# Kernel optimization log

Measured on AMD Instinct MI355X. Metric: run time of the kernel, lower is better.

The kernel has to match this reference:

```python
import jax, jax.numpy as jnp
import numpy as np

EPS = 1e-5

def _ln(x, g, b):
    mu = jnp.mean(x, -1, keepdims=True)
    var = jnp.mean(jnp.square(x - mu), -1, keepdims=True)
    return (x - mu) * jax.lax.rsqrt(var + EPS) * g + b

def _switch_moe(h, gw, gb, W1, b1, W2, b2):
    # h: [B,T,D]; top-1 switch routing over E experts
    probs = jax.nn.softmax(h @ gw + gb, axis=-1)        # [B,T,E]
    idx = jnp.argmax(probs, axis=-1)                    # [B,T]
    p = jnp.max(probs, axis=-1)[..., None]              # [B,T,1] top-1 gate prob
    out = jnp.zeros_like(h)
    E = W1.shape[0]
    for e in range(E):  # small fixed expert count
        y = jax.nn.gelu(h @ W1[e] + b1[e]) @ W2[e] + b2[e]
        out = out + jnp.where((idx == e)[..., None], p * y, 0.0)
    return out

def setup_inputs() -> dict:
    key = jax.random.key(0)
    B, T, D, F, E, TE, NB = 64, 196, 512, 2048, 8, 512, 2
    ks = jax.random.split(key, 16)
    s = 0.02
    return {
        "x": jax.random.normal(ks[0], (B, T, D), jnp.float32),
        "emb": jax.random.normal(ks[1], (B, TE), jnp.float32),
        "ln_g": jnp.ones((NB, D), jnp.float32),
        "ln_b": jnp.zeros((NB, D), jnp.float32),
        "gate_w": jax.random.normal(ks[2], (NB, D, E), jnp.float32) * s,
        "gate_b": jnp.zeros((NB, E), jnp.float32),
        "w1": jax.random.normal(ks[3], (NB, E, D, F), jnp.float32) * s,
        "b1": jnp.zeros((NB, E, F), jnp.float32),
        "w2": jax.random.normal(ks[4], (NB, E, F, D), jnp.float32) * s,
        "b2": jnp.zeros((NB, E, D), jnp.float32),
        "emb_w": jax.random.normal(ks[5], (TE, 2 * D), jnp.float32) * s,
        "emb_b": jnp.zeros((2 * D,), jnp.float32),
        "sn_g": jnp.ones((D,), jnp.float32),
        "sn_b": jnp.zeros((D,), jnp.float32),
        "out_w": jax.random.normal(ks[6], (D, D), jnp.float32) * s,
        "out_b": jnp.zeros((D,), jnp.float32),
    }

def reference(x, emb, ln_g, ln_b, gate_w, gate_b, w1, b1, w2, b2,
              emb_w, emb_b, sn_g, sn_b, out_w, out_b):
    NB = ln_g.shape[0]
    out = jnp.zeros_like(x)
    for br in range(NB):  # fixed small branch count; dropout = identity (eval)
        h = _ln(x, ln_g[br], ln_b[br])
        out = out + _switch_moe(h, gate_w[br], gate_b[br], w1[br], b1[br], w2[br], b2[br])
    out = out / NB
    # StylizationBlock (FiLM): norm, scale/shift from time emb, SiLU+Linear, residual
    eo = jax.nn.silu(emb) @ emb_w + emb_b            # [B,2D]
    scale, shift = jnp.split(eo[:, None, :], 2, axis=-1)  # [B,1,D] each
    h = _ln(out, sn_g, sn_b) * (1.0 + scale) + shift
    h = jax.nn.silu(h) @ out_w + out_b
    return x + h
```

## Files before the change

### kernel.cpp

```cpp
#include <hip/hip_runtime.h>
#include <hip/hip_bf16.h>

typedef unsigned short u16;
typedef unsigned int u32;

typedef short bf16v8 __attribute__((ext_vector_type(8)));
typedef float f32v4 __attribute__((ext_vector_type(4)));

constexpr int BB   = 64;
constexpr int TT   = 196;
constexpr int NTOK = BB * TT;
constexpr int DD   = 512;
constexpr int FF   = 2048;
constexpr int EE   = 8;
constexpr int NBR  = 2;
constexpr int GE   = NBR * EE;
constexpr int MT128 = 212;
constexpr int NB_FRONT = 8320 + NTOK / 4;

__device__ __forceinline__ u16 f2bf(float f) {
    union { float f; u32 u; } v; v.f = f;
    u32 r = v.u + 0x7fffu + ((v.u >> 16) & 1u);
    return (u16)(r >> 16);
}

__device__ __forceinline__ float bf2f(u32 u) {
    union { u32 u; float f; } v; v.u = u << 16; return v.f;
}

__device__ __forceinline__ float wave_sum(float v) {
    #pragma unroll
    for (int m = 32; m > 0; m >>= 1) v += __shfl_xor(v, m, 64);
    return v;
}

__device__ __forceinline__ float gelu_tanh(float v) {
    float y = 1.595769122f * v + 0.071354816f * (v * v * v);
    return v / (1.0f + __expf(-y));
}

__device__ __forceinline__ float silu(float v) {
    return v / (1.0f + __expf(-v));
}

__device__ __forceinline__ void gload16(const u16* g, u16* l) {
    typedef const __attribute__((address_space(1))) unsigned gv_t;
    typedef __attribute__((address_space(3))) unsigned lv_t;
    __builtin_amdgcn_global_load_lds((gv_t*)g, (lv_t*)l, 16, 0, 0);
}

__device__ __forceinline__ void bar() {
    asm volatile("" ::: "memory");
    __builtin_amdgcn_s_barrier();
    asm volatile("" ::: "memory");
}

#define ASM_VMCNT4 asm volatile("s_waitcnt vmcnt(4)" ::: "memory")
#define ASM_VMCNT0 asm volatile("s_waitcnt vmcnt(0)" ::: "memory")
#define ASM_LGKM0  asm volatile("s_waitcnt lgkmcnt(0)" ::: "memory")

__global__ __launch_bounds__(256) void front_kernel(
    const float* __restrict__ w1, u16* __restrict__ w1t,
    const float* __restrict__ w2, u16* __restrict__ w2t,
    const float* __restrict__ ow, u16* __restrict__ owt,
    const float* __restrict__ emb, const float* __restrict__ emb_w,
    const float* __restrict__ emb_b, float* __restrict__ eo,
    int* __restrict__ cnt,
    const float* __restrict__ x, const float* __restrict__ ln_g,
    const float* __restrict__ ln_b, const float* __restrict__ gate_w,
    const float* __restrict__ gate_b,
    u16* __restrict__ hA, u16* __restrict__ hB,
    int* __restrict__ idxb, float* __restrict__ pbuf)
{
    __shared__ float tile[64][69];
    __shared__ float se[4][DD];
    int id = blockIdx.x;
    int t = threadIdx.x;

    if (id >= 8320) {
        int wave = t >> 6, lane = t & 63;
        int tok = (id - 8320) * 4 + wave;
        const float* xr = x + (size_t)tok * DD + lane * 8;
        float4 v0 = *(const float4*)xr;
        float4 v1 = *(const float4*)(xr + 4);
        float xs[8] = {v0.x, v0.y, v0.z, v0.w, v1.x, v1.y, v1.z, v1.w};
        float s = 0.f, ss = 0.f;
        #pragma unroll
        for (int i = 0; i < 8; ++i) { s += xs[i]; ss += xs[i] * xs[i]; }
        s = wave_sum(s); ss = wave_sum(ss);
        float mu = s * (1.0f / DD);
        float var = ss * (1.0f / DD) - mu * mu;
        float rstd = rsqrtf(var + 1e-5f);

        #pragma unroll
        for (int br = 0; br < NBR; ++br) {
            u16* hb = br ? hB : hA;
            float part[8] = {0, 0, 0, 0, 0, 0, 0, 0};
            u16 hu[8];
            #pragma unroll
            for (int i = 0; i < 8; ++i) {
                int d = lane * 8 + i;
                float g = ln_g[br * DD + d], b = ln_b[br * DD + d];
                float h = (xs[i] - mu) * rstd * g + b;
                hu[i] = f2bf(h);
                const float* gw = gate_w + ((size_t)br * DD + d) * EE;
                float4 g0 = *(const float4*)gw;
                float4 g1 = *(const float4*)(gw + 4);
                part[0] += h * g0.x; part[1] += h * g0.y; part[2] += h * g0.z; part[3] += h * g0.w;
                part[4] += h * g1.x; part[5] += h * g1.y; part[6] += h * g1.z; part[7] += h * g1.w;
            }
            uint4 pk;
            pk.x = (u32)hu[0] | ((u32)hu[1] << 16);
            pk.y = (u32)hu[2] | ((u32)hu[3] << 16);
            pk.z = (u32)hu[4] | ((u32)hu[5] << 16);
            pk.w = (u32)hu[6] | ((u32)hu[7] << 16);
            *(uint4*)(hb + (size_t)tok * DD + lane * 8) = pk;

            float logit[8];
            #pragma unroll
            for (int e = 0; e < 8; ++e)
                logit[e] = wave_sum(part[e]) + gate_b[br * EE + e];
            float m = logit[0]; int bi = 0;
            #pragma unroll
            for (int e = 1; e < 8; ++e)
                if (logit[e] > m) { m = logit[e]; bi = e; }
            float sum = 0.f;
            #pragma unroll
            for (int e = 0; e < 8; ++e) sum += __expf(logit[e] - m);
            if (lane == 0) {
                idxb[br * NTOK + tok] = bi;
                pbuf[br * NTOK + tok] = 1.0f / sum;
            }
        }
        return;
    }

    if (id >= 8256) {
        int id2 = id - 8256;
        int cg = id2 & 3, bg = id2 >> 2;
        int b0 = bg * 4;
        int c0 = cg * 256 + t;
        for (int i = t; i < 4 * DD; i += 256) {
            int b = i >> 9, d = i & (DD - 1);
            se[b][d] = silu(emb[(size_t)(b0 + b) * DD + d]);
        }
        __syncthreads();
        float acc[4] = {0, 0, 0, 0};
        for (int k = 0; k < DD; ++k) {
            float wv = emb_w[(size_t)k * 1024 + c0];
            #pragma unroll
            for (int b = 0; b < 4; ++b) acc[b] += se[b][k] * wv;
        }
        float bb = emb_b[c0];
        #pragma unroll
        for (int b = 0; b < 4; ++b)
            eo[(size_t)(b0 + b) * 1024 + c0] = acc[b] + bb;
        return;
    }

    if (id == 0 && t < 16) cnt[t] = 0;

    const float* src; u16* dst; int R, C, rt, ct;
    if (id < 4096) {
        int e = id >> 8, rem = id & 255;
        R = DD; C = FF; rt = rem >> 5; ct = rem & 31;
        src = w1 + (size_t)e * R * C; dst = w1t + (size_t)e * R * C;
    } else if (id < 8192) {
        int e = (id - 4096) >> 8, rem = (id - 4096) & 255;
        R = FF; C = DD; rt = rem >> 3; ct = rem & 7;
        src = w2 + (size_t)e * R * C; dst = w2t + (size_t)e * R * C;
    } else {
        int rem = id - 8192;
        R = DD; C = DD; rt = rem >> 3; ct = rem & 7;
        src = ow; dst = owt;
    }
    int tx = t & 15, ty = t >> 4;
    int r0 = rt * 64, c0 = ct * 64;
    #pragma unroll
    for (int j = 0; j < 4; ++j) {
        int row = ty + j * 16;
        float4 v = *(const float4*)&src[(size_t)(r0 + row) * C + c0 + tx * 4];
        tile[row][tx * 4 + 0] = v.x;
        tile[row][tx * 4 + 1] = v.y;
        tile[row][tx * 4 + 2] = v.z;
        tile[row][tx * 4 + 3] = v.w;
    }
    __syncthreads();
    int wc = t & 7, wr0 = t >> 3;
    #pragma unroll
    for (int p = 0; p < 2; ++p) {
        int cc = wr0 + p * 32;
        u16 pk[8];
        #pragma unroll
        for (int i = 0; i < 8; ++i)
            pk[i] = f2bf(tile[wc * 8 + i][cc]);
        uint4 v;
        v.x = (u32)pk[0] | ((u32)pk[1] << 16);
        v.y = (u32)pk[2] | ((u32)pk[3] << 16);
        v.z = (u32)pk[4] | ((u32)pk[5] << 16);
        v.w = (u32)pk[6] | ((u32)pk[7] << 16);
        *(uint4*)&dst[(size_t)(c0 + cc) * R + r0 + wc * 8] = v;
    }
}

__global__ __launch_bounds__(256) void route_kernel(
    const int* __restrict__ idxb, int* __restrict__ cnt, int* __restrict__ list)
{
    __shared__ int lcnt[GE];
    __shared__ int gbase[GE];
    int tid = threadIdx.x;
    int t = blockIdx.x * 256 + tid;
    if (tid < GE) lcnt[tid] = 0;
    __syncthreads();
    int e0 = idxb[t];
    int e1 = EE + idxb[NTOK + t];
    int r0 = atomicAdd(&lcnt[e0], 1);
    int r1 = atomicAdd(&lcnt[e1], 1);
    __syncthreads();
    if (tid < GE) {
        int c = lcnt[tid];
        gbase[tid] = c ? atomicAdd(&cnt[tid], c) : 0;
    }
    __syncthreads();
    list[(size_t)e0 * NTOK + gbase[e0] + r0] = t;
    list[(size_t)e1 * NTOK + gbase[e1] + r1] = t;
}

__global__ void tilestart_kernel(const int* __restrict__ cnt, int* __restrict__ meta)
{
    int lane = threadIdx.x;
    if (lane < 16) {
        int pbv = 0;
        for (int k = 0; k < lane; ++k) pbv += cnt[k];
        meta[lane] = pbv;
    }
    if (lane == 16) {
        int n = 0;
        for (int k = 0; k < 16; ++k) n += (cnt[k] + 127) >> 7;
        meta[33] = n;
    }
    for (int j = lane; j < MT128; j += 64) {
        int ge = -1, start = 0, tt = 0;
        #pragma unroll
        for (int k = 0; k < 16; ++k) {
            int mt = (cnt[k] + 127) >> 7;
            if (ge < 0) {
                if (j < start + mt) { ge = k; tt = j - start; }
                else start += mt;
            }
        }
        if (ge >= 0) meta[64 + j] = (ge << 20) | tt;
    }
}

template<int MODE>
__global__ __launch_bounds__(256, 4) void gemm_tile(
    const u16* __restrict__ A0, const u16* __restrict__ A1,
    const u16* __restrict__ Bt,
    const int* __restrict__ meta, const int* __restrict__ cnt,
    const int* __restrict__ list, const float* __restrict__ pbuf,
    const float* __restrict__ bias,
    u16* __restrict__ uout, u16* __restrict__ moeout)
{
    constexpr int K = (MODE == 1) ? FF : DD;
    constexpr int N = (MODE == 0) ? FF : DD;
    constexpr int NSTEP = K / 32;

    __shared__ __align__(16) u16 As[2][128 * 32];
    __shared__ __align__(16) u16 Bs[2][128 * 32];
    __shared__ int rowtok[128];
    __shared__ float rowp[128];

    int ntile = blockIdx.x;
    int j = blockIdx.y;
    if (j >= meta[33]) return;
    int ev = meta[64 + j];
    int ge = ev >> 20;
    int rb = (ev & 0xfffff) << 7;
    int cnt_e = cnt[ge];
    int pb = meta[ge];

    int tid = threadIdx.x, wave = tid >> 6, lane = tid & 63;
    int wm = wave >> 1, wn = wave & 1;
    int fr = lane & 15, fq = lane >> 4;
    int r0 = wave * 16 + (lane >> 2);
    int sc = (lane & 3) ^ ((lane >> 3) & 3);

    const u16* Abase;
    if constexpr (MODE == 0) Abase = (ge >= 8) ? A1 : A0;
    else                     Abase = A0;
    const u16* Bte = Bt + (size_t)ge * FF * DD;

    const u16 *aSrc0, *aSrc1, *bSrc0, *bSrc1;
    if constexpr (MODE == 0) {
        int lb = ge * NTOK;
        int g0 = rb + r0, g1 = g0 + 64;
        int t0 = (g0 < cnt_e) ? list[lb + g0] : list[lb];
        int t1 = (g1 < cnt_e) ? list[lb + g1] : list[lb];
        aSrc0 = Abase + (size_t)t0 * K + sc * 8;
        aSrc1 = Abase + (size_t)t1 * K + sc * 8;
    } else {
        size_t base = (size_t)(pb + rb);
        aSrc0 = Abase + (base + r0) * (size_t)K + sc * 8;
        aSrc1 = Abase + (base + r0 + 64) * (size_t)K + sc * 8;
    }
    {
        int nrow = ntile * 128 + r0;
        bSrc0 = Bte + (size_t)nrow * K + sc * 8;
        bSrc1 = Bte + (size_t)(nrow + 64) * K + sc * 8;
    }

    if constexpr (MODE == 1) {
        if (tid < 128) {
            int g = rb + tid;
            int tk = (g < cnt_e) ? list[ge * NTOK + g] : -1;
            rowtok[tid] = tk;
            rowp[tid] = (tk >= 0) ? pbuf[(ge >> 3) * NTOK + tk] : 0.f;
        }
        ASM_LGKM0;
    }

    f32v4 acc[4][4];
    #pragma unroll
    for (int mi = 0; mi < 4; ++mi)
        #pragma unroll
        for (int ni = 0; ni < 4; ++ni)
            acc[mi][ni] = (f32v4){0.f, 0.f, 0.f, 0.f};

    int ch = fq ^ ((fr >> 1) & 3);

    gload16(aSrc0, &As[0][wave * 512]);
    gload16(aSrc1, &As[0][2048 + wave * 512]);
    gload16(bSrc0, &Bs[0][wave * 512]);
    gload16(bSrc1, &Bs[0][2048 + wave * 512]);
    aSrc0 += 32; aSrc1 += 32; bSrc0 += 32; bSrc1 += 32;

    #pragma unroll 2
    for (int t = 0; t < NSTEP; ++t) {
        const int cur = t & 1;
        if (t + 1 < NSTEP) {
            gload16(aSrc0, &As[cur ^ 1][wave * 512]);
            gload16(aSrc1, &As[cur ^ 1][2048 + wave * 512]);
            gload16(bSrc0, &Bs[cur ^ 1][wave * 512]);
            gload16(bSrc1, &Bs[cur ^ 1][2048 + wave * 512]);
            aSrc0 += 32; aSrc1 += 32; bSrc0 += 32; bSrc1 += 32;
            ASM_VMCNT4;
        } else {
            ASM_VMCNT0;
        }
        bar();

        bf16v8 af[4], bfr[4];
        #pragma unroll
        for (int mi = 0; mi < 4; ++mi)
            af[mi] = *(const bf16v8*)&As[cur][(wm * 64 + mi * 16 + fr) * 32 + ch * 8];
        #pragma unroll
        for (int ni = 0; ni < 4; ++ni)
            bfr[ni] = *(const bf16v8*)&Bs[cur][(wn * 64 + ni * 16 + fr) * 32 + ch * 8];
        #pragma unroll
        for (int mi = 0; mi < 4; ++mi)
            #pragma unroll
            for (int ni = 0; ni < 4; ++ni)
                acc[mi][ni] = __builtin_amdgcn_mfma_f32_16x16x32_bf16(
                    af[mi], bfr[ni], acc[mi][ni], 0, 0, 0);
        bar();
    }

    #pragma unroll
    for (int mi = 0; mi < 4; ++mi) {
        #pragma unroll
        for (int ni = 0; ni < 4; ++ni) {
            int col = ntile * 128 + wn * 64 + ni * 16 + fr;
            float bn = bias[(size_t)ge * N + col];
            #pragma unroll
            for (int r = 0; r < 4; ++r) {
                int rr = wm * 64 + mi * 16 + fq * 4 + r;
                float v = acc[mi][ni][r] + bn;
                if constexpr (MODE == 0) {
                    if (rb + rr < cnt_e)
                        uout[(size_t)(pb + rb + rr) * FF + col] = f2bf(gelu_tanh(v));
                } else {
                    int tok = rowtok[rr];
                    if (tok >= 0)
                        moeout[((size_t)(ge >> 3) * NTOK + tok) * DD + col] =
                            f2bf(v * rowp[rr]);
                }
            }
        }
    }
}

__global__ __launch_bounds__(256, 4) void gemm_out(
    const u16* __restrict__ A0, const u16* __restrict__ Bt,
    const float* __restrict__ bias,
    const float* __restrict__ xres, float* __restrict__ dout)
{
    constexpr int K = DD;
    constexpr int NSTEP = K / 32;

    __shared__ __align__(16) u16 As[2][128 * 32];
    __shared__ __align__(16) u16 Bs[2][128 * 32];

    int ntile = blockIdx.x;
    int rb = blockIdx.y * 128;

    int tid = threadIdx.x, wave = tid >> 6, lane = tid & 63;
    int wm = wave >> 1, wn = wave & 1;
    int fr = lane & 15, fq = lane >> 4;
    int r0 = wave * 16 + (lane >> 2);
    int sc = (lane & 3) ^ ((lane >> 3) & 3);

    const u16 *aSrc0, *aSrc1, *bSrc0, *bSrc1;
    aSrc0 = A0 + (size_t)(rb + r0) * K + sc * 8;
    aSrc1 = A0 + (size_t)(rb + r0 + 64) * K + sc * 8;
    {
        int nrow = ntile * 128 + r0;
        bSrc0 = Bt + (size_t)nrow * K + sc * 8;
        bSrc1 = Bt + (size_t)(nrow + 64) * K + sc * 8;
    }

    f32v4 acc[4][4];
    #pragma unroll
    for (int mi = 0; mi < 4; ++mi)
        #pragma unroll
        for (int ni = 0; ni < 4; ++ni)
            acc[mi][ni] = (f32v4){0.f, 0.f, 0.f, 0.f};

    int ch = fq ^ ((fr >> 1) & 3);

    gload16(aSrc0, &As[0][wave * 512]);
    gload16(aSrc1, &As[0][2048 + wave * 512]);
    gload16(bSrc0, &Bs[0][wave * 512]);
    gload16(bSrc1, &Bs[0][2048 + wave * 512]);
    aSrc0 += 32; aSrc1 += 32; bSrc0 += 32; bSrc1 += 32;

    #pragma unroll 2
    for (int t = 0; t < NSTEP; ++t) {
        const int cur = t & 1;
        if (t + 1 < NSTEP) {
            gload16(aSrc0, &As[cur ^ 1][wave * 512]);
            gload16(aSrc1, &As[cur ^ 1][2048 + wave * 512]);
            gload16(bSrc0, &Bs[cur ^ 1][wave * 512]);
            gload16(bSrc1, &Bs[cur ^ 1][2048 + wave * 512]);
            aSrc0 += 32; aSrc1 += 32; bSrc0 += 32; bSrc1 += 32;
            ASM_VMCNT4;
        } else {
            ASM_VMCNT0;
        }
        bar();

        bf16v8 af[4], bfr[4];
        #pragma unroll
        for (int mi = 0; mi < 4; ++mi)
            af[mi] = *(const bf16v8*)&As[cur][(wm * 64 + mi * 16 + fr) * 32 + ch * 8];
        #pragma unroll
        for (int ni = 0; ni < 4; ++ni)
            bfr[ni] = *(const bf16v8*)&Bs[cur][(wn * 64 + ni * 16 + fr) * 32 + ch * 8];
        #pragma unroll
        for (int mi = 0; mi < 4; ++mi)
            #pragma unroll
            for (int ni = 0; ni < 4; ++ni)
                acc[mi][ni] = __builtin_amdgcn_mfma_f32_16x16x32_bf16(
                    af[mi], bfr[ni], acc[mi][ni], 0, 0, 0);
        bar();
    }

    #pragma unroll
    for (int mi = 0; mi < 4; ++mi) {
        #pragma unroll
        for (int ni = 0; ni < 4; ++ni) {
            int col = ntile * 128 + wn * 64 + ni * 16 + fr;
            float bn = bias[col];
            #pragma unroll
            for (int r = 0; r < 4; ++r) {
                int rr = wm * 64 + mi * 16 + fq * 4 + r;
                size_t o = (size_t)(rb + rr) * DD + col;
                dout[o] = xres[o] + acc[mi][ni][r] + bn;
            }
        }
    }
}

__global__ __launch_bounds__(256) void stylize_kernel(
    const u16* __restrict__ moe, const float* __restrict__ eo,
    const float* __restrict__ sn_g, const float* __restrict__ sn_b,
    u16* __restrict__ sbuf)
{
    int wave = threadIdx.x >> 6, lane = threadIdx.x & 63;
    int tok = blockIdx.x * 4 + wave;
    int b = tok / TT;
    const u16* mr = moe + (size_t)tok * DD + lane * 8;
    const u16* mr2 = mr + (size_t)NTOK * DD;
    uint4 pa = *(const uint4*)mr;
    uint4 pb = *(const uint4*)mr2;
    float os[8];
    os[0] = (bf2f(pa.x & 0xffff) + bf2f(pb.x & 0xffff)) * 0.5f;
    os[1] = (bf2f(pa.x >> 16)    + bf2f(pb.x >> 16))    * 0.5f;
    os[2] = (bf2f(pa.y & 0xffff) + bf2f(pb.y & 0xffff)) * 0.5f;
    os[3] = (bf2f(pa.y >> 16)    + bf2f(pb.y >> 16))    * 0.5f;
    os[4] = (bf2f(pa.z & 0xffff) + bf2f(pb.z & 0xffff)) * 0.5f;
    os[5] = (bf2f(pa.z >> 16)    + bf2f(pb.z >> 16))    * 0.5f;
    os[6] = (bf2f(pa.w & 0xffff) + bf2f(pb.w & 0xffff)) * 0.5f;
    os[7] = (bf2f(pa.w >> 16)    + bf2f(pb.w >> 16))    * 0.5f;
    float s = 0.f, ss = 0.f;
    #pragma unroll
    for (int i = 0; i < 8; ++i) { s += os[i]; ss += os[i] * os[i]; }
    s = wave_sum(s); ss = wave_sum(ss);
    float mu = s * (1.0f / DD);
    float var = ss * (1.0f / DD) - mu * mu;
    float rstd = rsqrtf(var + 1e-5f);
    u16 hu[8];
    #pragma unroll
    for (int i = 0; i < 8; ++i) {
        int d = lane * 8 + i;
        float h = (os[i] - mu) * rstd * sn_g[d] + sn_b[d];
        float scv = eo[(size_t)b * 1024 + d];
        float shv = eo[(size_t)b * 1024 + DD + d];
        h = h * (1.0f + scv) + shv;
        hu[i] = f2bf(silu(h));
    }
    uint4 pk;
    pk.x = (u32)hu[0] | ((u32)hu[1] << 16);
    pk.y = (u32)hu[2] | ((u32)hu[3] << 16);
    pk.z = (u32)hu[4] | ((u32)hu[5] << 16);
    pk.w = (u32)hu[6] | ((u32)hu[7] << 16);
    *(uint4*)(sbuf + (size_t)tok * DD + lane * 8) = pk;
}

extern "C" void kernel_launch(void* const* d_in, const int* in_sizes, int n_in,
                              void* d_out, int out_size, void* d_ws, size_t ws_size,
                              hipStream_t stream)
{
    const float* x      = (const float*)d_in[0];
    const float* emb    = (const float*)d_in[1];
    const float* ln_g   = (const float*)d_in[2];
    const float* ln_b   = (const float*)d_in[3];
    const float* gate_w = (const float*)d_in[4];
    const float* gate_b = (const float*)d_in[5];
    const float* w1     = (const float*)d_in[6];
    const float* b1     = (const float*)d_in[7];
    const float* w2     = (const float*)d_in[8];
    const float* b2     = (const float*)d_in[9];
    const float* emb_w  = (const float*)d_in[10];
    const float* emb_b  = (const float*)d_in[11];
    const float* sn_g   = (const float*)d_in[12];
    const float* sn_b   = (const float*)d_in[13];
    const float* out_w  = (const float*)d_in[14];
    const float* out_b  = (const float*)d_in[15];
    (void)n_in; (void)in_sizes; (void)out_size; (void)ws_size;

    const size_t szW    = (size_t)GE * FF * DD * 2;
    const size_t szOwt  = (size_t)DD * DD * 2;
    const size_t szH    = (size_t)NTOK * DD * 2;
    const size_t szEo   = (size_t)BB * 2 * DD * 4;
    const size_t szP    = (size_t)NBR * NTOK * 4;
    const size_t szCnt  = 256, szMeta = 4096;
    const size_t szList = (size_t)GE * NTOK * 4;
    const size_t szU    = ((size_t)2 * NTOK + 256) * FF * 2;
    const size_t szM    = (size_t)2 * NTOK * DD * 2;

    auto align256 = [](size_t v) { return (v + 255) & ~(size_t)255; };
    char* w = (char*)d_ws;
    size_t off = 0;
    auto take = [&](size_t bytes) -> void* {
        void* p = w + off;
        off = align256(off + bytes);
        return p;
    };
    u16*   w1t  = (u16*)take(szW);
    u16*   w2t  = (u16*)take(szW);
    u16*   owt  = (u16*)take(szOwt);
    u16*   hA   = (u16*)take(szH);
    u16*   hB   = (u16*)take(szH);
    float* eo   = (float*)take(szEo);
    float* pbuf = (float*)take(szP);
    int*   idxb = (int*)take(szP);
    int*   cnt  = (int*)take(szCnt);
    int*   meta = (int*)take(szMeta);
    int*   list = (int*)take(szList);
    u16*   ubuf = (u16*)take(szU);
    u16*   moe  = (u16*)take(szM);

    front_kernel<<<NB_FRONT, 256, 0, stream>>>(w1, w1t, w2, w2t, out_w, owt,
                                               emb, emb_w, emb_b, eo, cnt,
                                               x, ln_g, ln_b, gate_w, gate_b,
                                               hA, hB, idxb, pbuf);

    route_kernel<<<NTOK / 256, 256, 0, stream>>>(idxb, cnt, list);
    tilestart_kernel<<<1, 64, 0, stream>>>(cnt, meta);

    gemm_tile<0><<<dim3(FF / 128, MT128), 256, 0, stream>>>(
        hA, hB, w1t, meta, cnt, list, nullptr, b1, ubuf, nullptr);
    gemm_tile<1><<<dim3(DD / 128, MT128), 256, 0, stream>>>(
        ubuf, nullptr, w2t, meta, cnt, list, pbuf, b2, nullptr, moe);

    stylize_kernel<<<NTOK / 4, 256, 0, stream>>>(moe, eo, sn_g, sn_b, hA);
    gemm_out<<<dim3(DD / 128, NTOK / 128), 256, 0, stream>>>(
        hA, owt, out_b, x, (float*)d_out);
}
```

Baseline: 339.2 us.

## Process multiple weight-transpose tiles per block with double-buffered LDS prefetch

The weight fp32→bf16 transpose in the front kernel now gives each block a 64-column strip and loops over 8 or 16 row tiles, instead of launching one block per 64x64 tile. This cuts the grid from about 8.3k transpose blocks to 776. The next tile's global loads are issued before the current tile is converted and stored, and the tiles alternate between two LDS buffers. The shared arrays are merged into one aliased buffer to fit the double buffer. The aim is to reduce block launch overhead and hide load latency, at the cost of less parallelism per block, which could leave some CUs idle.

After: 332.4 us. -2.0%, faster.

```diff
diff --git a/kernel.cpp b/kernel.cpp
--- a/kernel.cpp
+++ b/kernel.cpp
@@ -16,7 +16,7 @@
 constexpr int NBR  = 2;
 constexpr int GE   = NBR * EE;
 constexpr int MT128 = 212;
-constexpr int NB_FRONT = 8320 + NTOK / 4;
+constexpr int NB_FRONT = 840 + NTOK / 4;
 
 __device__ __forceinline__ u16 f2bf(float f) {
     union { float f; u32 u; } v; v.f = f;
@@ -72,14 +72,13 @@
     u16* __restrict__ hA, u16* __restrict__ hB,
     int* __restrict__ idxb, float* __restrict__ pbuf)
 {
-    __shared__ float tile[64][69];
-    __shared__ float se[4][DD];
+    __shared__ __align__(16) float smem[2 * 64 * 69];
     int id = blockIdx.x;
     int t = threadIdx.x;
 
-    if (id >= 8320) {
+    if (id >= 840) {
         int wave = t >> 6, lane = t & 63;
-        int tok = (id - 8320) * 4 + wave;
+        int tok = (id - 840) * 4 + wave;
         const float* xr = x + (size_t)tok * DD + lane * 8;
         float4 v0 = *(const float4*)xr;
         float4 v1 = *(const float4*)(xr + 4);
@@ -135,21 +134,22 @@
         return;
     }
 
-    if (id >= 8256) {
-        int id2 = id - 8256;
+    if (id >= 776) {
+        float* se = smem;
+        int id2 = id - 776;
         int cg = id2 & 3, bg = id2 >> 2;
         int b0 = bg * 4;
         int c0 = cg * 256 + t;
         for (int i = t; i < 4 * DD; i += 256) {
             int b = i >> 9, d = i & (DD - 1);
-            se[b][d] = silu(emb[(size_t)(b0 + b) * DD + d]);
+            se[b * DD + d] = silu(emb[(size_t)(b0 + b) * DD + d]);
         }
         __syncthreads();
         float acc[4] = {0, 0, 0, 0};
         for (int k = 0; k < DD; ++k) {
             float wv = emb_w[(size_t)k * 1024 + c0];
             #pragma unroll
-            for (int b = 0; b < 4; ++b) acc[b] += se[b][k] * wv;
+            for (int b = 0; b < 4; ++b) acc[b] += se[b * DD + k] * wv;
         }
         float bb = emb_b[c0];
         #pragma unroll
@@ -160,46 +160,75 @@
 
     if (id == 0 && t < 16) cnt[t] = 0;
 
-    const float* src; u16* dst; int R, C, rt, ct;
-    if (id < 4096) {
-        int e = id >> 8, rem = id & 255;
-        R = DD; C = FF; rt = rem >> 5; ct = rem & 31;
-        src = w1 + (size_t)e * R * C; dst = w1t + (size_t)e * R * C;
-    } else if (id < 8192) {
-        int e = (id - 4096) >> 8, rem = (id - 4096) & 255;
-        R = FF; C = DD; rt = rem >> 3; ct = rem & 7;
-        src = w2 + (size_t)e * R * C; dst = w2t + (size_t)e * R * C;
+    const float* src; u16* dst; int C, Rfull, rowbase, c0, NIT;
+    if (id < 512) {
+        int e = id >> 5, cg = id & 31;
+        src = w1 + (size_t)e * DD * FF; dst = w1t + (size_t)e * FF * DD;
+        C = FF; Rfull = DD; rowbase = 0; c0 = cg * 64; NIT = 8;
+    } else if (id < 768) {
+        int sid = id - 512; int e = sid >> 4, rem = sid & 15;
+        src = w2 + (size_t)e * FF * DD; dst = w2t + (size_t)e * FF * DD;
+        C = DD; Rfull = FF; rowbase = (rem >> 3) * 1024; c0 = (rem & 7) * 64; NIT = 16;
     } else {
-        int rem = id - 8192;
-        R = DD; C = DD; rt = rem >> 3; ct = rem & 7;
+        int cg = id - 768;
         src = ow; dst = owt;
-    }
+        C = DD; Rfull = DD; rowbase = 0; c0 = cg * 64; NIT = 8;
+    }
+
+    float (*tile)[64][69] = (float (*)[64][69])smem;
     int tx = t & 15, ty = t >> 4;
-    int r0 = rt * 64, c0 = ct * 64;
-    #pragma unroll
-    for (int j = 0; j < 4; ++j) {
-        int row = ty + j * 16;
-        float4 v = *(const float4*)&src[(size_t)(r0 + row) * C + c0 + tx * 4];
-        tile[row][tx * 4 + 0] = v.x;
-        tile[row][tx * 4 + 1] = v.y;
-        tile[row][tx * 4 + 2] = v.z;
-        tile[row][tx * 4 + 3] = v.w;
-    }
-    __syncthreads();
     int wc = t & 7, wr0 = t >> 3;
-    #pragma unroll
-    for (int p = 0; p < 2; ++p) {
-        int cc = wr0 + p * 32;
-        u16 pk[8];
-        #pragma unroll
-        for (int i = 0; i < 8; ++i)
-            pk[i] = f2bf(tile[wc * 8 + i][cc]);
-        uint4 v;
-        v.x = (u32)pk[0] | ((u32)pk[1] << 16);
-        v.y = (u32)pk[2] | ((u32)pk[3] << 16);
-        v.z = (u32)pk[4] | ((u32)pk[5] << 16);
-        v.w = (u32)pk[6] | ((u32)pk[7] << 16);
-        *(uint4*)&dst[(size_t)(c0 + cc) * R + r0 + wc * 8] = v;
+
+    {
+        float4 v[4];
+        #pragma unroll
+        for (int j = 0; j < 4; ++j)
+            v[j] = *(const float4*)&src[(size_t)(rowbase + ty + 16 * j) * C + c0 + tx * 4];
+        #pragma unroll
+        for (int j = 0; j < 4; ++j) {
+            int row = ty + 16 * j;
+            tile[0][row][tx * 4 + 0] = v[j].x;
+            tile[0][row][tx * 4 + 1] = v[j].y;
+            tile[0][row][tx * 4 + 2] = v[j].z;
+            tile[0][row][tx * 4 + 3] = v[j].w;
+        }
+        __syncthreads();
+    }
+
+    for (int it = 0; it < NIT; ++it) {
+        int cur = it & 1;
+        bool pre = (it + 1 < NIT);
+        float4 nv[4];
+        if (pre) {
+            #pragma unroll
+            for (int j = 0; j < 4; ++j)
+                nv[j] = *(const float4*)&src[(size_t)(rowbase + (it + 1) * 64 + ty + 16 * j) * C + c0 + tx * 4];
+        }
+        #pragma unroll
+        for (int p = 0; p < 2; ++p) {
+            int cc = wr0 + p * 32;
+            u16 pk[8];
+            #pragma unroll
+            for (int i = 0; i < 8; ++i)
+                pk[i] = f2bf(tile[cur][wc * 8 + i][cc]);
+            uint4 vv;
+            vv.x = (u32)pk[0] | ((u32)pk[1] << 16);
+            vv.y = (u32)pk[2] | ((u32)pk[3] << 16);
+            vv.z = (u32)pk[4] | ((u32)pk[5] << 16);
+            vv.w = (u32)pk[6] | ((u32)pk[7] << 16);
+            *(uint4*)&dst[(size_t)(c0 + cc) * Rfull + rowbase + it * 64 + wc * 8] = vv;
+        }
+        if (pre) {
+            #pragma unroll
+            for (int j = 0; j < 4; ++j) {
+                int row = ty + 16 * j;
+                tile[cur ^ 1][row][tx * 4 + 0] = nv[j].x;
+                tile[cur ^ 1][row][tx * 4 + 1] = nv[j].y;
+                tile[cur ^ 1][row][tx * 4 + 2] = nv[j].z;
+                tile[cur ^ 1][row][tx * 4 + 3] = nv[j].w;
+            }
+        }
+        __syncthreads();
     }
 }
 
```
